# Kernel optimization log

Measured on AMD Instinct MI355X. Metric: run time of the kernel, lower is better.

The kernel has to match this reference:

```python
import jax, jax.numpy as jnp
import numpy as np

HOP = 2
N_NODES = 50000
D_FEAT = 64
N_NNZ = 800000
N_QEDGES = 32768


def setup_inputs() -> dict:
    key = jax.random.key(0)
    k1, k2, k3, k4, k5 = jax.random.split(key, 5)
    x = jax.random.normal(k1, (N_NODES, D_FEAT), dtype=jnp.float32)
    # degrees must be strictly positive (reciprocal / rsqrt / sqrt applied)
    deg = 1.0 + 63.0 * jax.random.uniform(k2, (N_NODES, 1), dtype=jnp.float32)
    adj_row = jnp.sort(jax.random.randint(k3, (N_NNZ,), 0, N_NODES, dtype=jnp.int32))
    adj_col = jax.random.randint(k4, (N_NNZ,), 0, N_NODES, dtype=jnp.int32)
    edge = jax.random.randint(k5, (2, N_QEDGES), 0, N_NODES, dtype=jnp.int32)
    return {"x": x, "deg": deg, "adj_row": adj_row, "adj_col": adj_col, "edge": edge}


def reference(x, deg, adj_row, adj_col, edge):
    N, D = x.shape
    degrev = 1.0 / deg                      # [N,1]
    # fused degree feature expansion: [N, 3D]
    x3 = jnp.concatenate((x, x * jax.lax.rsqrt(deg), x * jnp.sqrt(deg)), axis=1)

    def spmm(v):  # unweighted adj_t @ v via gather + segment-sum
        return jax.ops.segment_sum(v[adj_col], adj_row, num_segments=N)

    xs = [x3, degrev * spmm(x3)]
    for _ in range(2, HOP + 1):  # Chebyshev-like recurrence
        xs.append(degrev * spmm(xs[-1]) - xs[-2])
    h = jnp.concatenate(xs, axis=1)              # [N, (hop+1)*3*D]
    h = h.reshape(N, 3 * (HOP + 1), D)           # unflatten(1, (-1, D))
    h = jnp.transpose(h, (0, 2, 1))              # [N, D, 3*(hop+1)]
    return h[edge]                               # [2, E_q, D, 3*(hop+1)]
```

## Files before the change

### kernel.cpp

```cpp
#include <hip/hip_runtime.h>

#define N_NODES 50000
#define D_FEAT 64
#define N_NNZ 800000
#define N_ENT 65536

typedef unsigned int uint32;
typedef unsigned short ushort16;

__device__ __forceinline__ uint32 rne1(float a) {
    uint32 u = __float_as_uint(a);
    return (u + 0x7FFFu + ((u >> 16) & 1u)) >> 16;
}
__device__ __forceinline__ uint32 rne2(float a, float b) {
    return rne1(a) | (rne1(b) << 16);
}
__device__ __forceinline__ float bf_lo(uint32 u) { return __uint_as_float(u << 16); }
__device__ __forceinline__ float bf_hi(uint32 u) { return __uint_as_float(u & 0xFFFF0000u); }
__device__ __forceinline__ void unpack8(const uint4 v, float* f) {
    f[0] = bf_lo(v.x); f[1] = bf_hi(v.x);
    f[2] = bf_lo(v.y); f[3] = bf_hi(v.y);
    f[4] = bf_lo(v.z); f[5] = bf_hi(v.z);
    f[6] = bf_lo(v.w); f[7] = bf_hi(v.w);
}
__device__ __forceinline__ float bf1(ushort16 u) { return __uint_as_float(((uint32)u) << 16); }

__global__ void build_rowptr_scal(const int* __restrict__ adj_row,
                                  const float* __restrict__ deg,
                                  int* __restrict__ row_ptr,
                                  float4* __restrict__ scal,
                                  int nnz, int n) {
    int r = blockIdx.x * blockDim.x + threadIdx.x;
    if (r > n) return;
    int lo = 0, hi = nnz;
    while (lo < hi) {
        int mid = (lo + hi) >> 1;
        if (adj_row[mid] < r) lo = mid + 1; else hi = mid;
    }
    row_ptr[r] = lo;
    if (r < n) {
        float d  = deg[r];
        float sq = sqrtf(d);
        scal[r] = make_float4(1.0f / d, 1.0f / sq, sq, 0.0f);
    }
}

__global__ __launch_bounds__(256) void pack_x(const float2* __restrict__ x2,
                                              uint32* __restrict__ xh, int npair) {
    int i = blockIdx.x * blockDim.x + threadIdx.x;
    if (i >= npair) return;
    float2 v = x2[i];
    xh[i] = rne2(v.x, v.y);
}

__global__ __launch_bounds__(256) void spmm1_kernel(
    const uint4* __restrict__ xh, const float4* __restrict__ scal,
    const int* __restrict__ adj_col, const int* __restrict__ row_ptr,
    uint4* __restrict__ y1h, int n) {
    int t    = threadIdx.x & 63;
    int f    = t & 7;
    int r    = (blockIdx.x * 4 + (threadIdx.x >> 6)) * 8 + (t >> 3);
    if (r >= n) return;

    int s = row_ptr[r], e = row_ptr[r + 1];
    int cnt = e - s;
    float a0[8], a1[8], a2[8];
#pragma unroll
    for (int j = 0; j < 8; ++j) { a0[j] = 0.f; a1[j] = 0.f; a2[j] = 0.f; }

    int i = 0;
    for (; i + 2 <= cnt; i += 2) {
        int c0 = adj_col[s + i];
        int c1 = adj_col[s + i + 1];
        uint4 xv0 = xh[(size_t)c0 * 8 + f];
        uint4 xv1 = xh[(size_t)c1 * 8 + f];
        float4 sc0 = scal[c0];
        float4 sc1 = scal[c1];
        float xf0[8], xf1[8];
        unpack8(xv0, xf0); unpack8(xv1, xf1);
#pragma unroll
        for (int j = 0; j < 8; ++j) {
            a0[j] += xf0[j];
            a1[j] += xf0[j] * sc0.y;
            a2[j] += xf0[j] * sc0.z;
            a0[j] += xf1[j];
            a1[j] += xf1[j] * sc1.y;
            a2[j] += xf1[j] * sc1.z;
        }
    }
    if (i < cnt) {
        int c = adj_col[s + i];
        uint4 xv = xh[(size_t)c * 8 + f];
        float4 sc = scal[c];
        float xf[8]; unpack8(xv, xf);
#pragma unroll
        for (int j = 0; j < 8; ++j) {
            a0[j] += xf[j];
            a1[j] += xf[j] * sc.y;
            a2[j] += xf[j] * sc.z;
        }
    }

    float dr = scal[r].x;
    uint4* yr = y1h + (size_t)r * 24 + f;
    yr[0]  = make_uint4(rne2(a0[0]*dr, a0[1]*dr), rne2(a0[2]*dr, a0[3]*dr),
                        rne2(a0[4]*dr, a0[5]*dr), rne2(a0[6]*dr, a0[7]*dr));
    yr[8]  = make_uint4(rne2(a1[0]*dr, a1[1]*dr), rne2(a1[2]*dr, a1[3]*dr),
                        rne2(a1[4]*dr, a1[5]*dr), rne2(a1[6]*dr, a1[7]*dr));
    yr[16] = make_uint4(rne2(a2[0]*dr, a2[1]*dr), rne2(a2[2]*dr, a2[3]*dr),
                        rne2(a2[4]*dr, a2[5]*dr), rne2(a2[6]*dr, a2[7]*dr));
}

__global__ __launch_bounds__(256) void spmm2_kernel(
    const float4* __restrict__ x4, const float4* __restrict__ scal,
    const int* __restrict__ adj_col, const int* __restrict__ row_ptr,
    const uint4* __restrict__ y1h, uint4* __restrict__ y2h, int n) {
    int t    = threadIdx.x & 63;
    int f    = t & 7;
    int r    = (blockIdx.x * 4 + (threadIdx.x >> 6)) * 8 + (t >> 3);
    if (r >= n) return;

    int s = row_ptr[r], e = row_ptr[r + 1];
    int cnt = e - s;
    float a0[8], a1[8], a2[8];
#pragma unroll
    for (int j = 0; j < 8; ++j) { a0[j] = 0.f; a1[j] = 0.f; a2[j] = 0.f; }

    int i = 0;
    for (; i + 2 <= cnt; i += 2) {
        int c0 = adj_col[s + i];
        int c1 = adj_col[s + i + 1];
        const uint4* yc0 = y1h + (size_t)c0 * 24 + f;
        const uint4* yc1 = y1h + (size_t)c1 * 24 + f;
        uint4 b0 = yc0[0], b1 = yc0[8], b2 = yc0[16];
        uint4 d0 = yc1[0], d1 = yc1[8], d2 = yc1[16];
        float f0[8], f1[8], f2[8], g0[8], g1[8], g2[8];
        unpack8(b0, f0); unpack8(b1, f1); unpack8(b2, f2);
        unpack8(d0, g0); unpack8(d1, g1); unpack8(d2, g2);
#pragma unroll
        for (int j = 0; j < 8; ++j) {
            a0[j] += f0[j] + g0[j];
            a1[j] += f1[j] + g1[j];
            a2[j] += f2[j] + g2[j];
        }
    }
    if (i < cnt) {
        int c = adj_col[s + i];
        const uint4* yc = y1h + (size_t)c * 24 + f;
        uint4 b0 = yc[0], b1 = yc[8], b2 = yc[16];
        float f0[8], f1[8], f2[8];
        unpack8(b0, f0); unpack8(b1, f1); unpack8(b2, f2);
#pragma unroll
        for (int j = 0; j < 8; ++j) {
            a0[j] += f0[j]; a1[j] += f1[j]; a2[j] += f2[j];
        }
    }

    float4 sc = scal[r];
    float4 xa = x4[(size_t)r * 16 + f * 2];
    float4 xb = x4[(size_t)r * 16 + f * 2 + 1];
    float xr[8] = {xa.x, xa.y, xa.z, xa.w, xb.x, xb.y, xb.z, xb.w};
    float v0[8], v1[8], v2[8];
#pragma unroll
    for (int j = 0; j < 8; ++j) {
        v0[j] = sc.x * a0[j] - xr[j];
        v1[j] = sc.x * a1[j] - xr[j] * sc.y;
        v2[j] = sc.x * a2[j] - xr[j] * sc.z;
    }
    uint4* yr = y2h + (size_t)r * 24 + f;
    yr[0]  = make_uint4(rne2(v0[0], v0[1]), rne2(v0[2], v0[3]),
                        rne2(v0[4], v0[5]), rne2(v0[6], v0[7]));
    yr[8]  = make_uint4(rne2(v1[0], v1[1]), rne2(v1[2], v1[3]),
                        rne2(v1[4], v1[5]), rne2(v1[6], v1[7]));
    yr[16] = make_uint4(rne2(v2[0], v2[1]), rne2(v2[2], v2[3]),
                        rne2(v2[4], v2[5]), rne2(v2[6], v2[7]));
}

__global__ __launch_bounds__(256) void gather_kernel(
    const float* __restrict__ x, const float4* __restrict__ scal,
    const int* __restrict__ edge, const ushort16* __restrict__ y1h,
    const ushort16* __restrict__ y2h, float* __restrict__ out) {
    __shared__ __align__(16) float lds[4][576];
    int wave = threadIdx.x >> 6;
    int t    = threadIdx.x & 63;
    int ent  = blockIdx.x * 4 + wave;

    int n = edge[ent];
    float4 sc = scal[n];
    float xv = x[n * D_FEAT + t];
    const ushort16* y1n = y1h + (size_t)n * 192;
    const ushort16* y2n = y2h + (size_t)n * 192;

    float h[9];
    h[0] = xv;              h[1] = xv * sc.y;        h[2] = xv * sc.z;
    h[3] = bf1(y1n[t]);     h[4] = bf1(y1n[64 + t]); h[5] = bf1(y1n[128 + t]);
    h[6] = bf1(y2n[t]);     h[7] = bf1(y2n[64 + t]); h[8] = bf1(y2n[128 + t]);

#pragma unroll
    for (int g = 0; g < 9; ++g) lds[wave][t * 9 + g] = h[g];
    __syncthreads();

    const float4* l4 = (const float4*)lds[wave];
    float4* o4 = (float4*)(out + (size_t)ent * 576);
    o4[t]      = l4[t];
    o4[t + 64] = l4[t + 64];
    if (t < 16) o4[t + 128] = l4[t + 128];
}

extern "C" void kernel_launch(void* const* d_in, const int* in_sizes, int n_in,
                              void* d_out, int out_size, void* d_ws, size_t ws_size,
                              hipStream_t stream) {
    const float* x       = (const float*)d_in[0];
    const float* deg     = (const float*)d_in[1];
    const int*   adj_row = (const int*)d_in[2];
    const int*   adj_col = (const int*)d_in[3];
    const int*   edge    = (const int*)d_in[4];
    float* out = (float*)d_out;

    char* ws = (char*)d_ws;
    size_t off = 0;
    int*    row_ptr = (int*)ws;            off = ((size_t)(N_NODES + 1) * 4 + 255) & ~(size_t)255;
    float4* scal    = (float4*)(ws + off); off += (size_t)N_NODES * 16;
    uint32* xh      = (uint32*)(ws + off); off += (size_t)N_NODES * 64 * 2;
    off = (off + 255) & ~(size_t)255;
    uint4*  y1h     = (uint4*)(ws + off);  off += (size_t)N_NODES * 192 * 2;
    off = (off + 255) & ~(size_t)255;
    uint4*  y2h     = (uint4*)(ws + off);

    build_rowptr_scal<<<(N_NODES + 1 + 255) / 256, 256, 0, stream>>>(
        adj_row, deg, row_ptr, scal, N_NNZ, N_NODES);
    pack_x<<<(N_NODES * 32 + 255) / 256, 256, 0, stream>>>(
        (const float2*)x, xh, N_NODES * 32);
    spmm1_kernel<<<(N_NODES + 31) / 32, 256, 0, stream>>>(
        (const uint4*)xh, scal, adj_col, row_ptr, y1h, N_NODES);
    spmm2_kernel<<<(N_NODES + 31) / 32, 256, 0, stream>>>(
        (const float4*)x, scal, adj_col, row_ptr, y1h, y2h, N_NODES);
    gather_kernel<<<N_ENT / 4, 256, 0, stream>>>(
        x, scal, edge, (const ushort16*)y1h, (const ushort16*)y2h, out);
}
```

Measured before the change: 257.2 us.

## Assign one wave per row in SpMM kernels with cross-lane shuffle reduction

Both SpMM kernels now map a whole 64-lane wave to a single row. The eight 8-lane groups stride over the row's nonzeros and their partial sums are combined with xor shuffles before lane group 0 writes the result. This aims to raise memory-level parallelism per row and remove serial per-row loops and imbalance between rows in a wave. In exchange it adds shuffle-reduction cost, and with short rows it leaves many lanes idle while launching 8x more blocks.

```diff
diff --git a/kernel.cpp b/kernel.cpp
--- a/kernel.cpp
+++ b/kernel.cpp
@@ -57,24 +57,25 @@
     const uint4* __restrict__ xh, const float4* __restrict__ scal,
     const int* __restrict__ adj_col, const int* __restrict__ row_ptr,
     uint4* __restrict__ y1h, int n) {
-    int t    = threadIdx.x & 63;
-    int f    = t & 7;
-    int r    = (blockIdx.x * 4 + (threadIdx.x >> 6)) * 8 + (t >> 3);
+    int t = threadIdx.x & 63;
+    int f = t & 7;
+    int o = t >> 3;
+    int r = blockIdx.x * 4 + (threadIdx.x >> 6);
     if (r >= n) return;
 
     int s = row_ptr[r], e = row_ptr[r + 1];
-    int cnt = e - s;
     float a0[8], a1[8], a2[8];
 #pragma unroll
     for (int j = 0; j < 8; ++j) { a0[j] = 0.f; a1[j] = 0.f; a2[j] = 0.f; }
 
-    int i = 0;
-    for (; i + 2 <= cnt; i += 2) {
-        int c0 = adj_col[s + i];
-        int c1 = adj_col[s + i + 1];
-        uint4 xv0 = xh[(size_t)c0 * 8 + f];
-        uint4 xv1 = xh[(size_t)c1 * 8 + f];
+    for (int i = s + o; i < e; i += 16) {
+        int  c0 = adj_col[i];
+        int  i1 = i + 8;
+        bool p1 = i1 < e;
+        int  c1 = adj_col[p1 ? i1 : i];
+        uint4  xv0 = xh[(size_t)c0 * 8 + f];
         float4 sc0 = scal[c0];
+        uint4  xv1 = xh[(size_t)c1 * 8 + f];
         float4 sc1 = scal[c1];
         float xf0[8], xf1[8];
         unpack8(xv0, xf0); unpack8(xv1, xf1);
@@ -83,53 +84,68 @@
             a0[j] += xf0[j];
             a1[j] += xf0[j] * sc0.y;
             a2[j] += xf0[j] * sc0.z;
-            a0[j] += xf1[j];
-            a1[j] += xf1[j] * sc1.y;
-            a2[j] += xf1[j] * sc1.z;
-        }
-    }
-    if (i < cnt) {
-        int c = adj_col[s + i];
-        uint4 xv = xh[(size_t)c * 8 + f];
-        float4 sc = scal[c];
-        float xf[8]; unpack8(xv, xf);
-#pragma unroll
-        for (int j = 0; j < 8; ++j) {
-            a0[j] += xf[j];
-            a1[j] += xf[j] * sc.y;
-            a2[j] += xf[j] * sc.z;
-        }
-    }
-
-    float dr = scal[r].x;
-    uint4* yr = y1h + (size_t)r * 24 + f;
-    yr[0]  = make_uint4(rne2(a0[0]*dr, a0[1]*dr), rne2(a0[2]*dr, a0[3]*dr),
-                        rne2(a0[4]*dr, a0[5]*dr), rne2(a0[6]*dr, a0[7]*dr));
-    yr[8]  = make_uint4(rne2(a1[0]*dr, a1[1]*dr), rne2(a1[2]*dr, a1[3]*dr),
-                        rne2(a1[4]*dr, a1[5]*dr), rne2(a1[6]*dr, a1[7]*dr));
-    yr[16] = make_uint4(rne2(a2[0]*dr, a2[1]*dr), rne2(a2[2]*dr, a2[3]*dr),
-                        rne2(a2[4]*dr, a2[5]*dr), rne2(a2[6]*dr, a2[7]*dr));
+        }
+        if (p1) {
+#pragma unroll
+            for (int j = 0; j < 8; ++j) {
+                a0[j] += xf1[j];
+                a1[j] += xf1[j] * sc1.y;
+                a2[j] += xf1[j] * sc1.z;
+            }
+        }
+    }
+
+#pragma unroll
+    for (int j = 0; j < 8; ++j) {
+        a0[j] += __shfl_xor(a0[j], 8);
+        a1[j] += __shfl_xor(a1[j], 8);
+        a2[j] += __shfl_xor(a2[j], 8);
+    }
+#pragma unroll
+    for (int j = 0; j < 8; ++j) {
+        a0[j] += __shfl_xor(a0[j], 16);
+        a1[j] += __shfl_xor(a1[j], 16);
+        a2[j] += __shfl_xor(a2[j], 16);
+    }
+#pragma unroll
+    for (int j = 0; j < 8; ++j) {
+        a0[j] += __shfl_xor(a0[j], 32);
+        a1[j] += __shfl_xor(a1[j], 32);
+        a2[j] += __shfl_xor(a2[j], 32);
+    }
+
+    if (t < 8) {
+        float dr = scal[r].x;
+        uint4* yr = y1h + (size_t)r * 24 + t;
+        yr[0]  = make_uint4(rne2(a0[0]*dr, a0[1]*dr), rne2(a0[2]*dr, a0[3]*dr),
+                            rne2(a0[4]*dr, a0[5]*dr), rne2(a0[6]*dr, a0[7]*dr));
+        yr[8]  = make_uint4(rne2(a1[0]*dr, a1[1]*dr), rne2(a1[2]*dr, a1[3]*dr),
+                            rne2(a1[4]*dr, a1[5]*dr), rne2(a1[6]*dr, a1[7]*dr));
+        yr[16] = make_uint4(rne2(a2[0]*dr, a2[1]*dr), rne2(a2[2]*dr, a2[3]*dr),
+                            rne2(a2[4]*dr, a2[5]*dr), rne2(a2[6]*dr, a2[7]*dr));
+    }
 }
 
 __global__ __launch_bounds__(256) void spmm2_kernel(
     const float4* __restrict__ x4, const float4* __restrict__ scal,
     const int* __restrict__ adj_col, const int* __restrict__ row_ptr,
     const uint4* __restrict__ y1h, uint4* __restrict__ y2h, int n) {
-    int t    = threadIdx.x & 63;
-    int f    = t & 7;
-    int r    = (blockIdx.x * 4 + (threadIdx.x >> 6)) * 8 + (t >> 3);
+    int t = threadIdx.x & 63;
+    int f = t & 7;
+    int o = t >> 3;
+    int r = blockIdx.x * 4 + (threadIdx.x >> 6);
     if (r >= n) return;
 
     int s = row_ptr[r], e = row_ptr[r + 1];
-    int cnt = e - s;
     float a0[8], a1[8], a2[8];
 #pragma unroll
     for (int j = 0; j < 8; ++j) { a0[j] = 0.f; a1[j] = 0.f; a2[j] = 0.f; }
 
-    int i = 0;
-    for (; i + 2 <= cnt; i += 2) {
-        int c0 = adj_col[s + i];
-        int c1 = adj_col[s + i + 1];
+    for (int i = s + o; i < e; i += 16) {
+        int  c0 = adj_col[i];
+        int  i1 = i + 8;
+        bool p1 = i1 < e;
+        int  c1 = adj_col[p1 ? i1 : i];
         const uint4* yc0 = y1h + (size_t)c0 * 24 + f;
         const uint4* yc1 = y1h + (size_t)c1 * 24 + f;
         uint4 b0 = yc0[0], b1 = yc0[8], b2 = yc0[16];
@@ -139,41 +155,59 @@
         unpack8(d0, g0); unpack8(d1, g1); unpack8(d2, g2);
 #pragma unroll
         for (int j = 0; j < 8; ++j) {
-            a0[j] += f0[j] + g0[j];
-            a1[j] += f1[j] + g1[j];
-            a2[j] += f2[j] + g2[j];
-        }
-    }
-    if (i < cnt) {
-        int c = adj_col[s + i];
-        const uint4* yc = y1h + (size_t)c * 24 + f;
-        uint4 b0 = yc[0], b1 = yc[8], b2 = yc[16];
-        float f0[8], f1[8], f2[8];
-        unpack8(b0, f0); unpack8(b1, f1); unpack8(b2, f2);
+            a0[j] += f0[j];
+            a1[j] += f1[j];
+            a2[j] += f2[j];
+        }
+        if (p1) {
+#pragma unroll
+            for (int j = 0; j < 8; ++j) {
+                a0[j] += g0[j];
+                a1[j] += g1[j];
+                a2[j] += g2[j];
+            }
+        }
+    }
+
+#pragma unroll
+    for (int j = 0; j < 8; ++j) {
+        a0[j] += __shfl_xor(a0[j], 8);
+        a1[j] += __shfl_xor(a1[j], 8);
+        a2[j] += __shfl_xor(a2[j], 8);
+    }
+#pragma unroll
+    for (int j = 0; j < 8; ++j) {
+        a0[j] += __shfl_xor(a0[j], 16);
+        a1[j] += __shfl_xor(a1[j], 16);
+        a2[j] += __shfl_xor(a2[j], 16);
+    }
+#pragma unroll
+    for (int j = 0; j < 8; ++j) {
+        a0[j] += __shfl_xor(a0[j], 32);
+        a1[j] += __shfl_xor(a1[j], 32);
+        a2[j] += __shfl_xor(a2[j], 32);
+    }
+
+    if (t < 8) {
+        float4 sc = scal[r];
+        float4 xa = x4[(size_t)r * 16 + t * 2];
+        float4 xb = x4[(size_t)r * 16 + t * 2 + 1];
+        float xr[8] = {xa.x, xa.y, xa.z, xa.w, xb.x, xb.y, xb.z, xb.w};
+        float v0[8], v1[8], v2[8];
 #pragma unroll
         for (int j = 0; j < 8; ++j) {
-            a0[j] += f0[j]; a1[j] += f1[j]; a2[j] += f2[j];
-        }
-    }
-
-    float4 sc = scal[r];
-    float4 xa = x4[(size_t)r * 16 + f * 2];
-    float4 xb = x4[(size_t)r * 16 + f * 2 + 1];
-    float xr[8] = {xa.x, xa.y, xa.z, xa.w, xb.x, xb.y, xb.z, xb.w};
-    float v0[8], v1[8], v2[8];
-#pragma unroll
-    for (int j = 0; j < 8; ++j) {
-        v0[j] = sc.x * a0[j] - xr[j];
-        v1[j] = sc.x * a1[j] - xr[j] * sc.y;
-        v2[j] = sc.x * a2[j] - xr[j] * sc.z;
-    }
-    uint4* yr = y2h + (size_t)r * 24 + f;
-    yr[0]  = make_uint4(rne2(v0[0], v0[1]), rne2(v0[2], v0[3]),
-                        rne2(v0[4], v0[5]), rne2(v0[6], v0[7]));
-    yr[8]  = make_uint4(rne2(v1[0], v1[1]), rne2(v1[2], v1[3]),
-                        rne2(v1[4], v1[5]), rne2(v1[6], v1[7]));
-    yr[16] = make_uint4(rne2(v2[0], v2[1]), rne2(v2[2], v2[3]),
-                        rne2(v2[4], v2[5]), rne2(v2[6], v2[7]));
+            v0[j] = sc.x * a0[j] - xr[j];
+            v1[j] = sc.x * a1[j] - xr[j] * sc.y;
+            v2[j] = sc.x * a2[j] - xr[j] * sc.z;
+        }
+        uint4* yr = y2h + (size_t)r * 24 + t;
+        yr[0]  = make_uint4(rne2(v0[0], v0[1]), rne2(v0[2], v0[3]),
+                            rne2(v0[4], v0[5]), rne2(v0[6], v0[7]));
+        yr[8]  = make_uint4(rne2(v1[0], v1[1]), rne2(v1[2], v1[3]),
+                            rne2(v1[4], v1[5]), rne2(v1[6], v1[7]));
+        yr[16] = make_uint4(rne2(v2[0], v2[1]), rne2(v2[2], v2[3]),
+                            rne2(v2[4], v2[5]), rne2(v2[6], v2[7]));
+    }
 }
 
 __global__ __launch_bounds__(256) void gather_kernel(
@@ -231,9 +265,9 @@
         adj_row, deg, row_ptr, scal, N_NNZ, N_NODES);
     pack_x<<<(N_NODES * 32 + 255) / 256, 256, 0, stream>>>(
         (const float2*)x, xh, N_NODES * 32);
-    spmm1_kernel<<<(N_NODES + 31) / 32, 256, 0, stream>>>(
+    spmm1_kernel<<<(N_NODES + 3) / 4, 256, 0, stream>>>(
         (const uint4*)xh, scal, adj_col, row_ptr, y1h, N_NODES);
-    spmm2_kernel<<<(N_NODES + 31) / 32, 256, 0, stream>>>(
+    spmm2_kernel<<<(N_NODES + 3) / 4, 256, 0, stream>>>(
         (const float4*)x, scal, adj_col, row_ptr, y1h, y2h, N_NODES);
     gather_kernel<<<N_ENT / 4, 256, 0, stream>>>(
         x, scal, edge, (const ushort16*)y1h, (const ushort16*)y2h, out);
```

Result: slower. 276.5 us (+7.5%).

## Store y1/y2 as separate feature planes and split spmm2 across planes

Applied to the files above, without the earlier changes.

Changes the bf16 intermediates from interleaved [N,3,64] rows to three separate [N,64] planes. spmm2 then launches a grid dimension of 3, with each block handling one plane and four neighbors per iteration. A 3.2MB plane fits in cache better, each gather touches one 128B row per neighbor, and there are three times as many blocks for parallelism. In exchange, adj_col and row_ptr are read three times, and the gather kernel's reads are now spread across planes.

```diff
diff --git a/kernel.cpp b/kernel.cpp
--- a/kernel.cpp
+++ b/kernel.cpp
@@ -7,6 +7,9 @@
 
 typedef unsigned int uint32;
 typedef unsigned short ushort16;
+
+#define PLANE_U4 ((size_t)N_NODES * 8)
+#define PLANE_US ((size_t)N_NODES * 64)
 
 __device__ __forceinline__ uint32 rne1(float a) {
     uint32 u = __float_as_uint(a);
@@ -102,78 +105,68 @@
     }
 
     float dr = scal[r].x;
-    uint4* yr = y1h + (size_t)r * 24 + f;
-    yr[0]  = make_uint4(rne2(a0[0]*dr, a0[1]*dr), rne2(a0[2]*dr, a0[3]*dr),
-                        rne2(a0[4]*dr, a0[5]*dr), rne2(a0[6]*dr, a0[7]*dr));
-    yr[8]  = make_uint4(rne2(a1[0]*dr, a1[1]*dr), rne2(a1[2]*dr, a1[3]*dr),
-                        rne2(a1[4]*dr, a1[5]*dr), rne2(a1[6]*dr, a1[7]*dr));
-    yr[16] = make_uint4(rne2(a2[0]*dr, a2[1]*dr), rne2(a2[2]*dr, a2[3]*dr),
-                        rne2(a2[4]*dr, a2[5]*dr), rne2(a2[6]*dr, a2[7]*dr));
+    size_t base = (size_t)r * 8 + f;
+    y1h[base]               = make_uint4(rne2(a0[0]*dr, a0[1]*dr), rne2(a0[2]*dr, a0[3]*dr),
+                                         rne2(a0[4]*dr, a0[5]*dr), rne2(a0[6]*dr, a0[7]*dr));
+    y1h[base + PLANE_U4]    = make_uint4(rne2(a1[0]*dr, a1[1]*dr), rne2(a1[2]*dr, a1[3]*dr),
+                                         rne2(a1[4]*dr, a1[5]*dr), rne2(a1[6]*dr, a1[7]*dr));
+    y1h[base + 2*PLANE_U4]  = make_uint4(rne2(a2[0]*dr, a2[1]*dr), rne2(a2[2]*dr, a2[3]*dr),
+                                         rne2(a2[4]*dr, a2[5]*dr), rne2(a2[6]*dr, a2[7]*dr));
 }
 
 __global__ __launch_bounds__(256) void spmm2_kernel(
     const float4* __restrict__ x4, const float4* __restrict__ scal,
     const int* __restrict__ adj_col, const int* __restrict__ row_ptr,
     const uint4* __restrict__ y1h, uint4* __restrict__ y2h, int n) {
-    int t    = threadIdx.x & 63;
-    int f    = t & 7;
-    int r    = (blockIdx.x * 4 + (threadIdx.x >> 6)) * 8 + (t >> 3);
+    int t = threadIdx.x & 63;
+    int f = t & 7;
+    int r = (blockIdx.x * 4 + (threadIdx.x >> 6)) * 8 + (t >> 3);
+    int g = blockIdx.y;
     if (r >= n) return;
+    const uint4* yp = y1h + (size_t)g * PLANE_U4;
 
     int s = row_ptr[r], e = row_ptr[r + 1];
     int cnt = e - s;
-    float a0[8], a1[8], a2[8];
-#pragma unroll
-    for (int j = 0; j < 8; ++j) { a0[j] = 0.f; a1[j] = 0.f; a2[j] = 0.f; }
+    float a[8];
+#pragma unroll
+    for (int j = 0; j < 8; ++j) a[j] = 0.f;
 
     int i = 0;
-    for (; i + 2 <= cnt; i += 2) {
+    for (; i + 4 <= cnt; i += 4) {
         int c0 = adj_col[s + i];
         int c1 = adj_col[s + i + 1];
-        const uint4* yc0 = y1h + (size_t)c0 * 24 + f;
-        const uint4* yc1 = y1h + (size_t)c1 * 24 + f;
-        uint4 b0 = yc0[0], b1 = yc0[8], b2 = yc0[16];
-        uint4 d0 = yc1[0], d1 = yc1[8], d2 = yc1[16];
-        float f0[8], f1[8], f2[8], g0[8], g1[8], g2[8];
-        unpack8(b0, f0); unpack8(b1, f1); unpack8(b2, f2);
-        unpack8(d0, g0); unpack8(d1, g1); unpack8(d2, g2);
-#pragma unroll
-        for (int j = 0; j < 8; ++j) {
-            a0[j] += f0[j] + g0[j];
-            a1[j] += f1[j] + g1[j];
-            a2[j] += f2[j] + g2[j];
-        }
-    }
-    if (i < cnt) {
+        int c2 = adj_col[s + i + 2];
+        int c3 = adj_col[s + i + 3];
+        uint4 b0 = yp[(size_t)c0 * 8 + f];
+        uint4 b1 = yp[(size_t)c1 * 8 + f];
+        uint4 b2 = yp[(size_t)c2 * 8 + f];
+        uint4 b3 = yp[(size_t)c3 * 8 + f];
+        float f0[8], f1[8], f2[8], f3[8];
+        unpack8(b0, f0); unpack8(b1, f1); unpack8(b2, f2); unpack8(b3, f3);
+#pragma unroll
+        for (int j = 0; j < 8; ++j)
+            a[j] += (f0[j] + f1[j]) + (f2[j] + f3[j]);
+    }
+    for (; i < cnt; ++i) {
         int c = adj_col[s + i];
-        const uint4* yc = y1h + (size_t)c * 24 + f;
-        uint4 b0 = yc[0], b1 = yc[8], b2 = yc[16];
-        float f0[8], f1[8], f2[8];
-        unpack8(b0, f0); unpack8(b1, f1); unpack8(b2, f2);
-#pragma unroll
-        for (int j = 0; j < 8; ++j) {
-            a0[j] += f0[j]; a1[j] += f1[j]; a2[j] += f2[j];
-        }
+        uint4 b = yp[(size_t)c * 8 + f];
+        float fv[8]; unpack8(b, fv);
+#pragma unroll
+        for (int j = 0; j < 8; ++j) a[j] += fv[j];
     }
 
     float4 sc = scal[r];
+    float w = (g == 0) ? 1.0f : ((g == 1) ? sc.y : sc.z);
     float4 xa = x4[(size_t)r * 16 + f * 2];
     float4 xb = x4[(size_t)r * 16 + f * 2 + 1];
     float xr[8] = {xa.x, xa.y, xa.z, xa.w, xb.x, xb.y, xb.z, xb.w};
-    float v0[8], v1[8], v2[8];
-#pragma unroll
-    for (int j = 0; j < 8; ++j) {
-        v0[j] = sc.x * a0[j] - xr[j];
-        v1[j] = sc.x * a1[j] - xr[j] * sc.y;
-        v2[j] = sc.x * a2[j] - xr[j] * sc.z;
-    }
-    uint4* yr = y2h + (size_t)r * 24 + f;
-    yr[0]  = make_uint4(rne2(v0[0], v0[1]), rne2(v0[2], v0[3]),
-                        rne2(v0[4], v0[5]), rne2(v0[6], v0[7]));
-    yr[8]  = make_uint4(rne2(v1[0], v1[1]), rne2(v1[2], v1[3]),
-                        rne2(v1[4], v1[5]), rne2(v1[6], v1[7]));
-    yr[16] = make_uint4(rne2(v2[0], v2[1]), rne2(v2[2], v2[3]),
-                        rne2(v2[4], v2[5]), rne2(v2[6], v2[7]));
+    float v[8];
+#pragma unroll
+    for (int j = 0; j < 8; ++j) v[j] = sc.x * a[j] - xr[j] * w;
+
+    uint4* yr = y2h + (size_t)g * PLANE_U4 + (size_t)r * 8 + f;
+    yr[0] = make_uint4(rne2(v[0], v[1]), rne2(v[2], v[3]),
+                       rne2(v[4], v[5]), rne2(v[6], v[7]));
 }
 
 __global__ __launch_bounds__(256) void gather_kernel(
@@ -188,13 +181,12 @@
     int n = edge[ent];
     float4 sc = scal[n];
     float xv = x[n * D_FEAT + t];
-    const ushort16* y1n = y1h + (size_t)n * 192;
-    const ushort16* y2n = y2h + (size_t)n * 192;
+    size_t nb = (size_t)n * 64 + t;
 
     float h[9];
-    h[0] = xv;              h[1] = xv * sc.y;        h[2] = xv * sc.z;
-    h[3] = bf1(y1n[t]);     h[4] = bf1(y1n[64 + t]); h[5] = bf1(y1n[128 + t]);
-    h[6] = bf1(y2n[t]);     h[7] = bf1(y2n[64 + t]); h[8] = bf1(y2n[128 + t]);
+    h[0] = xv;                      h[1] = xv * sc.y;                h[2] = xv * sc.z;
+    h[3] = bf1(y1h[nb]);            h[4] = bf1(y1h[nb + PLANE_US]);  h[5] = bf1(y1h[nb + 2*PLANE_US]);
+    h[6] = bf1(y2h[nb]);            h[7] = bf1(y2h[nb + PLANE_US]);  h[8] = bf1(y2h[nb + 2*PLANE_US]);
 
 #pragma unroll
     for (int g = 0; g < 9; ++g) lds[wave][t * 9 + g] = h[g];
@@ -227,13 +219,15 @@
     off = (off + 255) & ~(size_t)255;
     uint4*  y2h     = (uint4*)(ws + off);
 
+    int nblk = (N_NODES + 31) / 32;
+
     build_rowptr_scal<<<(N_NODES + 1 + 255) / 256, 256, 0, stream>>>(
         adj_row, deg, row_ptr, scal, N_NNZ, N_NODES);
     pack_x<<<(N_NODES * 32 + 255) / 256, 256, 0, stream>>>(
         (const float2*)x, xh, N_NODES * 32);
-    spmm1_kernel<<<(N_NODES + 31) / 32, 256, 0, stream>>>(
+    spmm1_kernel<<<nblk, 256, 0, stream>>>(
         (const uint4*)xh, scal, adj_col, row_ptr, y1h, N_NODES);
-    spmm2_kernel<<<(N_NODES + 31) / 32, 256, 0, stream>>>(
+    spmm2_kernel<<<dim3(nblk, 3), 256, 0, stream>>>(
         (const float4*)x, scal, adj_col, row_ptr, y1h, y2h, N_NODES);
     gather_kernel<<<N_ENT / 4, 256, 0, stream>>>(
         x, scal, edge, (const ushort16*)y1h, (const ushort16*)y2h, out);
```

Result: no change. 255.0 us (-0.8%).
